# Kernel optimization log

Hardware: AMD Instinct MI355X
Metric: run time of the kernel (lower is better)

Reference implementation:

```python
import jax, jax.numpy as jnp
import numpy as np

N = 50000       # nodes
E = 800000      # edges (avg degree 16)
NFEAT = 256
NHID = 32
NHEADS = 4
ALPHA = 0.2     # leaky relu slope


def setup_inputs() -> dict:
    key = jax.random.key(0)
    ks = jax.random.split(key, 7)
    x = jax.random.normal(ks[0], (N, NFEAT), dtype=jnp.float32)
    src = jax.random.randint(ks[1], (E,), 0, N, dtype=jnp.int32)
    dst = jax.random.randint(ks[2], (E,), 0, N, dtype=jnp.int32)
    Ws = jax.random.normal(ks[3], (NHEADS, NFEAT, NHID), dtype=jnp.float32) * 0.05
    As = jax.random.normal(ks[4], (NHEADS, 2 * NHID), dtype=jnp.float32) * 0.05
    Wo = jax.random.normal(ks[5], (NHID * NHEADS, NHID), dtype=jnp.float32) * 0.05
    Ao = jax.random.normal(ks[6], (2 * NHID,), dtype=jnp.float32) * 0.05
    return {"x": x, "src": src, "dst": dst, "Ws": Ws, "As": As, "Wo": Wo, "Ao": Ao}


def _gat_layer(h, src, dst, W, a, concat):
    # h: [N, F_in] -> project
    h = h @ W                          # [N, d]
    d = W.shape[1]
    hs = h[src]                        # [E, d] gather source feats
    hd = h[dst]                        # [E, d] gather neighbor feats
    # a . concat([hs, hd]) == hs @ a[:d] + hd @ a[d:]
    e = hs @ a[:d] + hd @ a[d:]        # [E]
    e = jnp.where(e > 0, e, ALPHA * e)  # leaky relu
    # segment softmax keyed on src
    m = jax.ops.segment_max(e, src, num_segments=N)    # [N]
    ex = jnp.exp(e - m[src])
    denom = jax.ops.segment_sum(ex, src, num_segments=N)  # [N]
    att = ex / denom[src]              # [E]
    # weighted neighbor aggregation (scatter-sum on src)
    h_prime = jax.ops.segment_sum(att[:, None] * hd, src, num_segments=N)  # [N, d]
    return jax.nn.elu(h_prime) if concat else h_prime


def reference(x, src, dst, Ws, As, Wo, Ao):
    heads = [_gat_layer(x, src, dst, Ws[i], As[i], concat=True) for i in range(NHEADS)]
    h = jnp.concatenate(heads, axis=1)                 # [N, nhid*nheads]
    out = jax.nn.elu(_gat_layer(h, src, dst, Wo, Ao, concat=False))  # [N, nhid]
    return out
```

## Files before the change

kernel.cpp:

```cpp
#include <hip/hip_runtime.h>
#include <hip/hip_fp16.h>
#include <math.h>

#define N_NODES 50000
#define N_EDGES 800000
#define NFEAT 256
#define NHID 32
#define NHEADS 4
#define ALPHA 0.2f
#define ELLCAP 64
#define ELLSH 6

typedef _Float16 half8_t __attribute__((ext_vector_type(8)));
typedef float f32x4 __attribute__((ext_vector_type(4)));

__device__ __forceinline__ float elu_f(float x) {
    return x > 0.0f ? x : (__expf(x) - 1.0f);
}

__device__ __forceinline__ float wexp(float x) {
    float l = x > 0.0f ? x : ALPHA * x;
    return __expf(l);
}

__global__ void k_prep(const float* __restrict__ Ws, const float* __restrict__ Wo,
                       ushort* __restrict__ Wt1, ushort* __restrict__ Wt2) {
    int idx = blockIdx.x * 256 + threadIdx.x;
    if (idx < 128 * 256) {
        int c = idx >> 8;
        int k = idx & 255;
        __half hv = __float2half(Ws[(c >> 5) * (NFEAT * NHID) + k * NHID + (c & 31)]);
        Wt1[idx] = *(ushort*)&hv;
    } else if (idx < 128 * 256 + 32 * 128) {
        int j = idx - 128 * 256;
        int c = j >> 7;
        int k = j & 127;
        __half hv = __float2half(Wo[k * NHID + c]);
        Wt2[j] = *(ushort*)&hv;
    }
}

template <int K, int NTILES, bool AHALF, int NH>
__global__ __launch_bounds__(256) void k_gemm_mfma(const void* __restrict__ Ain,
                                                   const ushort* __restrict__ Wt,
                                                   const float* __restrict__ attn,
                                                   __half* __restrict__ C,
                                                   float* __restrict__ So,
                                                   float* __restrict__ Si,
                                                   int nrows) {
    constexpr int N = NTILES * 16;
    constexpr int BK = 32;
    constexpr int LDB = 40;

    __shared__ __align__(16) ushort Bs[N * LDB];

    int tid = threadIdx.x;
    int w = tid >> 6;
    int lane = tid & 63;
    int c = lane & 15;
    int quad = lane >> 4;
    int row0 = blockIdx.x * 64 + w * 16;
    int gm = row0 + c;
    if (gm >= nrows) gm = nrows - 1;

    f32x4 acc[NTILES];
#pragma unroll
    for (int nt = 0; nt < NTILES; nt++)
#pragma unroll
        for (int i = 0; i < 4; i++) acc[nt][i] = 0.0f;

    float a_so[NTILES], a_si[NTILES];
#pragma unroll
    for (int nt = 0; nt < NTILES; nt++) {
        int h = nt >> 1;
        a_so[nt] = attn[h * 64 + (nt & 1) * 16 + c];
        a_si[nt] = attn[h * 64 + 32 + (nt & 1) * 16 + c];
    }

    for (int k0 = 0; k0 < K; k0 += BK) {
        if (tid < N * 2) {
            int r = tid >> 1;
            int part = tid & 1;
            const uint4* gp = (const uint4*)(Wt + (size_t)r * K + k0 + part * 16);
            uint4 v0 = gp[0];
            uint4 v1 = gp[1];
            uint4* lp = (uint4*)&Bs[r * LDB + part * 16];
            lp[0] = v0;
            lp[1] = v1;
        }
        __syncthreads();

        half8_t ahi, alo;
        if constexpr (AHALF) {
            ahi = *(const half8_t*)((const ushort*)Ain + (size_t)gm * K + k0 + quad * 8);
        } else {
            const float* ap = (const float*)Ain + (size_t)gm * K + k0 + quad * 8;
            float4 x0 = *(const float4*)ap;
            float4 x1 = *(const float4*)(ap + 4);
            float xa[8] = {x0.x, x0.y, x0.z, x0.w, x1.x, x1.y, x1.z, x1.w};
#pragma unroll
            for (int j = 0; j < 8; j++) {
                _Float16 h = (_Float16)xa[j];
                ahi[j] = h;
                alo[j] = (_Float16)(xa[j] - (float)h);
            }
        }
#pragma unroll
        for (int nt = 0; nt < NTILES; nt++) {
            half8_t b = *(const half8_t*)&Bs[(nt * 16 + c) * LDB + quad * 8];
            acc[nt] = __builtin_amdgcn_mfma_f32_16x16x32_f16(ahi, b, acc[nt], 0, 0, 0);
            if constexpr (!AHALF)
                acc[nt] = __builtin_amdgcn_mfma_f32_16x16x32_f16(alo, b, acc[nt], 0, 0, 0);
        }
        __syncthreads();
    }

#pragma unroll
    for (int reg = 0; reg < 4; reg++) {
        int ro = row0 + quad * 4 + reg;
        bool ok = ro < nrows;
        if (ok) {
#pragma unroll
            for (int nt = 0; nt < NTILES; nt++)
                C[(size_t)ro * N + nt * 16 + c] = __float2half(acc[nt][reg]);
        }
#pragma unroll
        for (int h = 0; h < NH; h++) {
            float so = acc[2 * h][reg] * a_so[2 * h] + acc[2 * h + 1][reg] * a_so[2 * h + 1];
            float si = acc[2 * h][reg] * a_si[2 * h] + acc[2 * h + 1][reg] * a_si[2 * h + 1];
            so += __shfl_xor(so, 1); si += __shfl_xor(si, 1);
            so += __shfl_xor(so, 2); si += __shfl_xor(si, 2);
            so += __shfl_xor(so, 4); si += __shfl_xor(si, 4);
            so += __shfl_xor(so, 8); si += __shfl_xor(si, 8);
            if (c == 0 && ok) {
                So[(size_t)ro * NH + h] = so;
                Si[(size_t)ro * NH + h] = si;
            }
        }
    }
}

__global__ void k_fill(const int* __restrict__ src, const int* __restrict__ dst,
                       int* __restrict__ deg, int* __restrict__ ell) {
    int e = blockIdx.x * 256 + threadIdx.x;
    if (e >= N_EDGES) return;
    int s = src[e];
    int v = dst[e];
    int slot = atomicAdd(&deg[s], 1);
    if (slot < ELLCAP) ell[((size_t)s << ELLSH) + slot] = v;
}

__global__ __launch_bounds__(256) void k_aggw4(const int* __restrict__ deg,
                                               const int* __restrict__ ell,
                                               const float* __restrict__ S1o,
                                               const float* __restrict__ S1i,
                                               const __half* __restrict__ H1h,
                                               __half* __restrict__ Hch) {
    int node = blockIdx.x * 4 + (threadIdx.x >> 6);
    if (node >= N_NODES) return;
    int lane = threadIdx.x & 63;
    int ha = lane >> 4;
    int dg = deg[node];
    if (dg > ELLCAP) dg = ELLCAP;
    const int* lp = ell + ((size_t)node << ELLSH);
    const unsigned* Hp = (const unsigned*)H1h;
    float so = S1o[node * 4 + ha];
    float a0 = 0.0f, a1 = 0.0f, d = 0.0f;
    int j = 0;
    for (; j + 1 < dg; j += 2) {
        int v0 = lp[j];
        int v1 = lp[j + 1];
        float w0 = wexp(so + S1i[4 * (size_t)v0 + ha]);
        float w1 = wexp(so + S1i[4 * (size_t)v1 + ha]);
        unsigned u0 = Hp[((size_t)v0 << 6) + lane];
        unsigned u1 = Hp[((size_t)v1 << 6) + lane];
        float2 h0 = __half22float2(*(__half2*)&u0);
        float2 h1 = __half22float2(*(__half2*)&u1);
        a0 += w0 * h0.x; a1 += w0 * h0.y; d += w0;
        a0 += w1 * h1.x; a1 += w1 * h1.y; d += w1;
    }
    if (j < dg) {
        int v0 = lp[j];
        float w0 = wexp(so + S1i[4 * (size_t)v0 + ha]);
        unsigned u0 = Hp[((size_t)v0 << 6) + lane];
        float2 h0 = __half22float2(*(__half2*)&u0);
        a0 += w0 * h0.x; a1 += w0 * h0.y; d += w0;
    }
    float inv = d > 0.0f ? 1.0f / d : 0.0f;
    __half2 o = __floats2half2_rn(elu_f(a0 * inv), elu_f(a1 * inv));
    *(__half2*)(Hch + ((size_t)node << 7) + 2 * lane) = o;
}

__global__ __launch_bounds__(256) void k_aggw2(const int* __restrict__ deg,
                                               const int* __restrict__ ell,
                                               const float* __restrict__ S2o,
                                               const float* __restrict__ S2i,
                                               const __half* __restrict__ H2h,
                                               float* __restrict__ out) {
    int t = blockIdx.x * 256 + threadIdx.x;
    int node = t >> 4;
    if (node >= N_NODES) return;
    int l = t & 15;
    int dg = deg[node];
    if (dg > ELLCAP) dg = ELLCAP;
    const int* lp = ell + ((size_t)node << ELLSH);
    const unsigned* Hp = (const unsigned*)H2h;
    float so = S2o[node];
    float a0 = 0.0f, a1 = 0.0f, d = 0.0f;
    int j = 0;
    for (; j + 1 < dg; j += 2) {
        int v0 = lp[j];
        int v1 = lp[j + 1];
        float w0 = wexp(so + S2i[v0]);
        float w1 = wexp(so + S2i[v1]);
        unsigned u0 = Hp[((size_t)v0 << 4) + l];
        unsigned u1 = Hp[((size_t)v1 << 4) + l];
        float2 h0 = __half22float2(*(__half2*)&u0);
        float2 h1 = __half22float2(*(__half2*)&u1);
        a0 += w0 * h0.x; a1 += w0 * h0.y; d += w0;
        a0 += w1 * h1.x; a1 += w1 * h1.y; d += w1;
    }
    if (j < dg) {
        int v0 = lp[j];
        float w0 = wexp(so + S2i[v0]);
        unsigned u0 = Hp[((size_t)v0 << 4) + l];
        float2 h0 = __half22float2(*(__half2*)&u0);
        a0 += w0 * h0.x; a1 += w0 * h0.y; d += w0;
    }
    float inv = d > 0.0f ? 1.0f / d : 0.0f;
    float2 o = make_float2(elu_f(a0 * inv), elu_f(a1 * inv));
    *(float2*)(out + ((size_t)node << 5) + 2 * l) = o;
}

extern "C" void kernel_launch(void* const* d_in, const int* in_sizes, int n_in,
                              void* d_out, int out_size, void* d_ws, size_t ws_size,
                              hipStream_t stream) {
    const float* x = (const float*)d_in[0];
    const int* src = (const int*)d_in[1];
    const int* dst = (const int*)d_in[2];
    const float* Ws = (const float*)d_in[3];
    const float* As = (const float*)d_in[4];
    const float* Wo = (const float*)d_in[5];
    const float* Ao = (const float*)d_in[6];
    float* out = (float*)d_out;

    char* p = (char*)d_ws;
    auto alloc = [&](size_t bytes) -> void* {
        void* r = (void*)p;
        p += (bytes + 255) & ~(size_t)255;
        return r;
    };
    ushort* Wt1 = (ushort*)alloc((size_t)128 * 256 * 2);
    ushort* Wt2 = (ushort*)alloc((size_t)32 * 128 * 2);
    __half* H1h = (__half*)alloc((size_t)N_NODES * 128 * 2);
    __half* Hch = (__half*)alloc((size_t)N_NODES * 128 * 2);
    __half* H2h = (__half*)alloc((size_t)N_NODES * 32 * 2);
    float* S1o = (float*)alloc((size_t)N_NODES * 4 * 4);
    float* S1i = (float*)alloc((size_t)N_NODES * 4 * 4);
    float* S2o = (float*)alloc((size_t)N_NODES * 4);
    float* S2i = (float*)alloc((size_t)N_NODES * 4);
    int* deg   = (int*)alloc((size_t)N_NODES * 4);
    int* ell   = (int*)alloc((size_t)N_NODES * ELLCAP * 4);

    const int EDGE_BLKS = (N_EDGES + 255) / 256;
    const int GEMM_BLKS = (N_NODES + 63) / 64;

    hipMemsetAsync(deg, 0, (size_t)N_NODES * 4, stream);

    k_prep<<<(128 * 256 + 32 * 128 + 255) / 256, 256, 0, stream>>>(Ws, Wo, Wt1, Wt2);

    k_gemm_mfma<256, 8, false, 4><<<GEMM_BLKS, 256, 0, stream>>>(
        x, Wt1, As, H1h, S1o, S1i, N_NODES);

    k_fill<<<EDGE_BLKS, 256, 0, stream>>>(src, dst, deg, ell);

    k_aggw4<<<(N_NODES + 3) / 4, 256, 0, stream>>>(deg, ell, S1o, S1i, H1h, Hch);

    k_gemm_mfma<128, 2, true, 1><<<GEMM_BLKS, 256, 0, stream>>>(
        Hch, Wt2, Ao, H2h, S2o, S2i, N_NODES);

    k_aggw2<<<(N_NODES * 16 + 255) / 256, 256, 0, stream>>>(deg, ell, S2o, S2i, H2h, out);
}
```

Measured before the change: 242.2 us.

## Precompute per-edge attention weights in fill pass, store with neighbor in ELL

The fill kernel now computes the four layer-1 attention exponentials per edge, packed as halves, and stores them next to the neighbor index in a 16-byte ELL entry. A new edge pass does the same for layer 2, writing into the reused H1h buffer. Both aggregation kernels then read the weights directly instead of gathering S*i and calling exp for each neighbor, and their loops unroll by 4. In exchange the ELL footprint grows (16B and 8B per entry), an extra edge kernel and an eslot array are added, and the layer-1 weights drop to half precision.

Measured after the change: 243.7 us. About the same (+0.6%).

```diff
diff --git a/kernel.cpp b/kernel.cpp
--- a/kernel.cpp
+++ b/kernel.cpp
@@ -21,6 +21,11 @@
 __device__ __forceinline__ float wexp(float x) {
     float l = x > 0.0f ? x : ALPHA * x;
     return __expf(l);
+}
+
+__device__ __forceinline__ float h2f_bits(unsigned wd, int sh) {
+    ushort b = (ushort)(wd >> sh);
+    return __half2float(*(__half*)&b);
 }
 
 __global__ void k_prep(const float* __restrict__ Ws, const float* __restrict__ Wo,
@@ -141,48 +146,70 @@
 }
 
 __global__ void k_fill(const int* __restrict__ src, const int* __restrict__ dst,
-                       int* __restrict__ deg, int* __restrict__ ell) {
+                       const float* __restrict__ S1o, const float* __restrict__ S1i,
+                       int* __restrict__ deg, uint4* __restrict__ ell16,
+                       int* __restrict__ eslot) {
     int e = blockIdx.x * 256 + threadIdx.x;
     if (e >= N_EDGES) return;
     int s = src[e];
     int v = dst[e];
     int slot = atomicAdd(&deg[s], 1);
-    if (slot < ELLCAP) ell[((size_t)s << ELLSH) + slot] = v;
+    eslot[e] = slot;
+    if (slot >= ELLCAP) return;
+    float4 so = *(const float4*)(S1o + 4 * (size_t)s);
+    float4 si = *(const float4*)(S1i + 4 * (size_t)v);
+    __half2 w01 = __floats2half2_rn(wexp(so.x + si.x), wexp(so.y + si.y));
+    __half2 w23 = __floats2half2_rn(wexp(so.z + si.z), wexp(so.w + si.w));
+    uint4 q;
+    q.x = (unsigned)v;
+    q.y = *(unsigned*)&w01;
+    q.z = *(unsigned*)&w23;
+    q.w = 0;
+    ell16[((size_t)s << ELLSH) + slot] = q;
 }
 
 __global__ __launch_bounds__(256) void k_aggw4(const int* __restrict__ deg,
-                                               const int* __restrict__ ell,
-                                               const float* __restrict__ S1o,
-                                               const float* __restrict__ S1i,
+                                               const uint4* __restrict__ ell16,
                                                const __half* __restrict__ H1h,
                                                __half* __restrict__ Hch) {
     int node = blockIdx.x * 4 + (threadIdx.x >> 6);
     if (node >= N_NODES) return;
     int lane = threadIdx.x & 63;
     int ha = lane >> 4;
+    int sel = ha & 2;
+    int sh = (ha & 1) * 16;
     int dg = deg[node];
     if (dg > ELLCAP) dg = ELLCAP;
-    const int* lp = ell + ((size_t)node << ELLSH);
+    const uint4* lp = ell16 + ((size_t)node << ELLSH);
     const unsigned* Hp = (const unsigned*)H1h;
-    float so = S1o[node * 4 + ha];
     float a0 = 0.0f, a1 = 0.0f, d = 0.0f;
     int j = 0;
-    for (; j + 1 < dg; j += 2) {
-        int v0 = lp[j];
-        int v1 = lp[j + 1];
-        float w0 = wexp(so + S1i[4 * (size_t)v0 + ha]);
-        float w1 = wexp(so + S1i[4 * (size_t)v1 + ha]);
-        unsigned u0 = Hp[((size_t)v0 << 6) + lane];
-        unsigned u1 = Hp[((size_t)v1 << 6) + lane];
+    for (; j + 3 < dg; j += 4) {
+        uint4 q0 = lp[j];
+        uint4 q1 = lp[j + 1];
+        uint4 q2 = lp[j + 2];
+        uint4 q3 = lp[j + 3];
+        unsigned u0 = Hp[((size_t)q0.x << 6) + lane];
+        unsigned u1 = Hp[((size_t)q1.x << 6) + lane];
+        unsigned u2 = Hp[((size_t)q2.x << 6) + lane];
+        unsigned u3 = Hp[((size_t)q3.x << 6) + lane];
+        float w0 = h2f_bits(sel ? q0.z : q0.y, sh);
+        float w1 = h2f_bits(sel ? q1.z : q1.y, sh);
+        float w2 = h2f_bits(sel ? q2.z : q2.y, sh);
+        float w3 = h2f_bits(sel ? q3.z : q3.y, sh);
         float2 h0 = __half22float2(*(__half2*)&u0);
         float2 h1 = __half22float2(*(__half2*)&u1);
+        float2 h2 = __half22float2(*(__half2*)&u2);
+        float2 h3 = __half22float2(*(__half2*)&u3);
         a0 += w0 * h0.x; a1 += w0 * h0.y; d += w0;
         a0 += w1 * h1.x; a1 += w1 * h1.y; d += w1;
-    }
-    if (j < dg) {
-        int v0 = lp[j];
-        float w0 = wexp(so + S1i[4 * (size_t)v0 + ha]);
-        unsigned u0 = Hp[((size_t)v0 << 6) + lane];
+        a0 += w2 * h2.x; a1 += w2 * h2.y; d += w2;
+        a0 += w3 * h3.x; a1 += w3 * h3.y; d += w3;
+    }
+    for (; j < dg; j++) {
+        uint4 q0 = lp[j];
+        unsigned u0 = Hp[((size_t)q0.x << 6) + lane];
+        float w0 = h2f_bits(sel ? q0.z : q0.y, sh);
         float2 h0 = __half22float2(*(__half2*)&u0);
         a0 += w0 * h0.x; a1 += w0 * h0.y; d += w0;
     }
@@ -191,10 +218,25 @@
     *(__half2*)(Hch + ((size_t)node << 7) + 2 * lane) = o;
 }
 
+__global__ void k_w2fill(const int* __restrict__ src, const int* __restrict__ dst,
+                         const int* __restrict__ eslot,
+                         const float* __restrict__ S2o, const float* __restrict__ S2i,
+                         uint2* __restrict__ ew2) {
+    int e = blockIdx.x * 256 + threadIdx.x;
+    if (e >= N_EDGES) return;
+    int s = src[e];
+    int v = dst[e];
+    int slot = eslot[e];
+    if (slot >= ELLCAP) return;
+    float w = wexp(S2o[s] + S2i[v]);
+    uint2 q;
+    q.x = (unsigned)v;
+    q.y = __float_as_uint(w);
+    ew2[((size_t)s << ELLSH) + slot] = q;
+}
+
 __global__ __launch_bounds__(256) void k_aggw2(const int* __restrict__ deg,
-                                               const int* __restrict__ ell,
-                                               const float* __restrict__ S2o,
-                                               const float* __restrict__ S2i,
+                                               const uint2* __restrict__ ew2,
                                                const __half* __restrict__ H2h,
                                                float* __restrict__ out) {
     int t = blockIdx.x * 256 + threadIdx.x;
@@ -203,27 +245,36 @@
     int l = t & 15;
     int dg = deg[node];
     if (dg > ELLCAP) dg = ELLCAP;
-    const int* lp = ell + ((size_t)node << ELLSH);
+    const uint2* lp = ew2 + ((size_t)node << ELLSH);
     const unsigned* Hp = (const unsigned*)H2h;
-    float so = S2o[node];
     float a0 = 0.0f, a1 = 0.0f, d = 0.0f;
     int j = 0;
-    for (; j + 1 < dg; j += 2) {
-        int v0 = lp[j];
-        int v1 = lp[j + 1];
-        float w0 = wexp(so + S2i[v0]);
-        float w1 = wexp(so + S2i[v1]);
-        unsigned u0 = Hp[((size_t)v0 << 4) + l];
-        unsigned u1 = Hp[((size_t)v1 << 4) + l];
+    for (; j + 3 < dg; j += 4) {
+        uint2 q0 = lp[j];
+        uint2 q1 = lp[j + 1];
+        uint2 q2 = lp[j + 2];
+        uint2 q3 = lp[j + 3];
+        unsigned u0 = Hp[((size_t)q0.x << 4) + l];
+        unsigned u1 = Hp[((size_t)q1.x << 4) + l];
+        unsigned u2 = Hp[((size_t)q2.x << 4) + l];
+        unsigned u3 = Hp[((size_t)q3.x << 4) + l];
+        float w0 = __uint_as_float(q0.y);
+        float w1 = __uint_as_float(q1.y);
+        float w2 = __uint_as_float(q2.y);
+        float w3 = __uint_as_float(q3.y);
         float2 h0 = __half22float2(*(__half2*)&u0);
         float2 h1 = __half22float2(*(__half2*)&u1);
+        float2 h2 = __half22float2(*(__half2*)&u2);
+        float2 h3 = __half22float2(*(__half2*)&u3);
         a0 += w0 * h0.x; a1 += w0 * h0.y; d += w0;
         a0 += w1 * h1.x; a1 += w1 * h1.y; d += w1;
-    }
-    if (j < dg) {
-        int v0 = lp[j];
-        float w0 = wexp(so + S2i[v0]);
-        unsigned u0 = Hp[((size_t)v0 << 4) + l];
+        a0 += w2 * h2.x; a1 += w2 * h2.y; d += w2;
+        a0 += w3 * h3.x; a1 += w3 * h3.y; d += w3;
+    }
+    for (; j < dg; j++) {
+        uint2 q0 = lp[j];
+        unsigned u0 = Hp[((size_t)q0.x << 4) + l];
+        float w0 = __uint_as_float(q0.y);
         float2 h0 = __half22float2(*(__half2*)&u0);
         a0 += w0 * h0.x; a1 += w0 * h0.y; d += w0;
     }
@@ -254,13 +305,15 @@
     ushort* Wt2 = (ushort*)alloc((size_t)32 * 128 * 2);
     __half* H1h = (__half*)alloc((size_t)N_NODES * 128 * 2);
     __half* Hch = (__half*)alloc((size_t)N_NODES * 128 * 2);
+    uint2* ew2 = (uint2*)H1h;
     __half* H2h = (__half*)alloc((size_t)N_NODES * 32 * 2);
     float* S1o = (float*)alloc((size_t)N_NODES * 4 * 4);
     float* S1i = (float*)alloc((size_t)N_NODES * 4 * 4);
     float* S2o = (float*)alloc((size_t)N_NODES * 4);
     float* S2i = (float*)alloc((size_t)N_NODES * 4);
     int* deg   = (int*)alloc((size_t)N_NODES * 4);
-    int* ell   = (int*)alloc((size_t)N_NODES * ELLCAP * 4);
+    int* eslot = (int*)alloc((size_t)N_EDGES * 4);
+    uint4* ell16 = (uint4*)alloc((size_t)N_NODES * ELLCAP * 16);
 
     const int EDGE_BLKS = (N_EDGES + 255) / 256;
     const int GEMM_BLKS = (N_NODES + 63) / 64;
@@ -272,12 +325,14 @@
     k_gemm_mfma<256, 8, false, 4><<<GEMM_BLKS, 256, 0, stream>>>(
         x, Wt1, As, H1h, S1o, S1i, N_NODES);
 
-    k_fill<<<EDGE_BLKS, 256, 0, stream>>>(src, dst, deg, ell);
-
-    k_aggw4<<<(N_NODES + 3) / 4, 256, 0, stream>>>(deg, ell, S1o, S1i, H1h, Hch);
+    k_fill<<<EDGE_BLKS, 256, 0, stream>>>(src, dst, S1o, S1i, deg, ell16, eslot);
+
+    k_aggw4<<<(N_NODES + 3) / 4, 256, 0, stream>>>(deg, ell16, H1h, Hch);
 
     k_gemm_mfma<128, 2, true, 1><<<GEMM_BLKS, 256, 0, stream>>>(
         Hch, Wt2, Ao, H2h, S2o, S2i, N_NODES);
 
-    k_aggw2<<<(N_NODES * 16 + 255) / 256, 256, 0, stream>>>(deg, ell, S2o, S2i, H2h, out);
-}
+    k_w2fill<<<EDGE_BLKS, 256, 0, stream>>>(src, dst, eslot, S2o, S2i, ew2);
+
+    k_aggw2<<<(N_NODES * 16 + 255) / 256, 256, 0, stream>>>(deg, ew2, H2h, out);
+}
```

## Precompute per-edge attention weights into ELL-aligned buffers before aggregation

Applied to the files above, without the earlier changes.

Adds two per-slot kernels that compute the leaky-relu exp attention weights once per edge: packed fp16 for the four heads in layer 1, fp32 for layer 2. They are stored alongside the ELL neighbor list. The aggregation kernels then read neighbors and weights with vectorized 16-byte loads and unroll by four, no longer doing redundant per-lane score gathers and exps. The cost is two extra launches over all 64 slots per node, extra workspace traffic for the weight arrays, and fp16 rounding of the layer-1 weights.

Result: no change. 245.0 us (+1.2%).

```diff
diff --git a/kernel.cpp b/kernel.cpp
--- a/kernel.cpp
+++ b/kernel.cpp
@@ -21,6 +21,11 @@
 __device__ __forceinline__ float wexp(float x) {
     float l = x > 0.0f ? x : ALPHA * x;
     return __expf(l);
+}
+
+__device__ __forceinline__ float h2f_bits(unsigned wd, int sh) {
+    ushort b = (ushort)(wd >> sh);
+    return __half2float(*(__half*)&b);
 }
 
 __global__ void k_prep(const float* __restrict__ Ws, const float* __restrict__ Wo,
@@ -141,48 +146,82 @@
 }
 
 __global__ void k_fill(const int* __restrict__ src, const int* __restrict__ dst,
-                       int* __restrict__ deg, int* __restrict__ ell) {
+                       int* __restrict__ deg, int* __restrict__ ell4) {
     int e = blockIdx.x * 256 + threadIdx.x;
     if (e >= N_EDGES) return;
     int s = src[e];
     int v = dst[e];
     int slot = atomicAdd(&deg[s], 1);
-    if (slot < ELLCAP) ell[((size_t)s << ELLSH) + slot] = v;
+    if (slot < ELLCAP) ell4[((size_t)s << ELLSH) + slot] = v;
+}
+
+__global__ __launch_bounds__(256) void k_wfill1(const int* __restrict__ deg,
+                                                const int* __restrict__ ell4,
+                                                const float* __restrict__ S1o,
+                                                const float* __restrict__ S1i,
+                                                uint2* __restrict__ ellw8) {
+    int t = blockIdx.x * 256 + threadIdx.x;
+    int node = t >> ELLSH;
+    if (node >= N_NODES) return;
+    int slot = t & (ELLCAP - 1);
+    int dg = deg[node];
+    if (dg > ELLCAP) dg = ELLCAP;
+    if (slot >= dg) return;
+    int v = ell4[t];
+    float4 so = *(const float4*)(S1o + 4 * (size_t)node);
+    float4 si = *(const float4*)(S1i + 4 * (size_t)v);
+    __half2 w01 = __floats2half2_rn(wexp(so.x + si.x), wexp(so.y + si.y));
+    __half2 w23 = __floats2half2_rn(wexp(so.z + si.z), wexp(so.w + si.w));
+    uint2 q;
+    q.x = *(unsigned*)&w01;
+    q.y = *(unsigned*)&w23;
+    ellw8[t] = q;
 }
 
 __global__ __launch_bounds__(256) void k_aggw4(const int* __restrict__ deg,
-                                               const int* __restrict__ ell,
-                                               const float* __restrict__ S1o,
-                                               const float* __restrict__ S1i,
+                                               const int* __restrict__ ell4,
+                                               const uint2* __restrict__ ellw8,
                                                const __half* __restrict__ H1h,
                                                __half* __restrict__ Hch) {
     int node = blockIdx.x * 4 + (threadIdx.x >> 6);
     if (node >= N_NODES) return;
     int lane = threadIdx.x & 63;
     int ha = lane >> 4;
+    int sel = ha & 2;
+    int sh = (ha & 1) * 16;
     int dg = deg[node];
     if (dg > ELLCAP) dg = ELLCAP;
-    const int* lp = ell + ((size_t)node << ELLSH);
+    const uint4* dp = (const uint4*)(ell4 + ((size_t)node << ELLSH));
+    const uint4* wp = (const uint4*)(ellw8 + ((size_t)node << ELLSH));
     const unsigned* Hp = (const unsigned*)H1h;
-    float so = S1o[node * 4 + ha];
     float a0 = 0.0f, a1 = 0.0f, d = 0.0f;
     int j = 0;
-    for (; j + 1 < dg; j += 2) {
-        int v0 = lp[j];
-        int v1 = lp[j + 1];
-        float w0 = wexp(so + S1i[4 * (size_t)v0 + ha]);
-        float w1 = wexp(so + S1i[4 * (size_t)v1 + ha]);
-        unsigned u0 = Hp[((size_t)v0 << 6) + lane];
-        unsigned u1 = Hp[((size_t)v1 << 6) + lane];
+    for (; j + 3 < dg; j += 4) {
+        uint4 d4 = dp[j >> 2];
+        uint4 wA = wp[j >> 1];
+        uint4 wB = wp[(j >> 1) + 1];
+        unsigned u0 = Hp[((size_t)d4.x << 6) + lane];
+        unsigned u1 = Hp[((size_t)d4.y << 6) + lane];
+        unsigned u2 = Hp[((size_t)d4.z << 6) + lane];
+        unsigned u3 = Hp[((size_t)d4.w << 6) + lane];
+        float w0 = h2f_bits(sel ? wA.y : wA.x, sh);
+        float w1 = h2f_bits(sel ? wA.w : wA.z, sh);
+        float w2 = h2f_bits(sel ? wB.y : wB.x, sh);
+        float w3 = h2f_bits(sel ? wB.w : wB.z, sh);
         float2 h0 = __half22float2(*(__half2*)&u0);
         float2 h1 = __half22float2(*(__half2*)&u1);
+        float2 h2 = __half22float2(*(__half2*)&u2);
+        float2 h3 = __half22float2(*(__half2*)&u3);
         a0 += w0 * h0.x; a1 += w0 * h0.y; d += w0;
         a0 += w1 * h1.x; a1 += w1 * h1.y; d += w1;
-    }
-    if (j < dg) {
-        int v0 = lp[j];
-        float w0 = wexp(so + S1i[4 * (size_t)v0 + ha]);
+        a0 += w2 * h2.x; a1 += w2 * h2.y; d += w2;
+        a0 += w3 * h3.x; a1 += w3 * h3.y; d += w3;
+    }
+    for (; j < dg; j++) {
+        int v0 = ell4[((size_t)node << ELLSH) + j];
+        uint2 q0 = ellw8[((size_t)node << ELLSH) + j];
         unsigned u0 = Hp[((size_t)v0 << 6) + lane];
+        float w0 = h2f_bits(sel ? q0.y : q0.x, sh);
         float2 h0 = __half22float2(*(__half2*)&u0);
         a0 += w0 * h0.x; a1 += w0 * h0.y; d += w0;
     }
@@ -191,10 +230,25 @@
     *(__half2*)(Hch + ((size_t)node << 7) + 2 * lane) = o;
 }
 
+__global__ __launch_bounds__(256) void k_wfill2(const int* __restrict__ deg,
+                                                const int* __restrict__ ell4,
+                                                const float* __restrict__ S2o,
+                                                const float* __restrict__ S2i,
+                                                float* __restrict__ ew2) {
+    int t = blockIdx.x * 256 + threadIdx.x;
+    int node = t >> ELLSH;
+    if (node >= N_NODES) return;
+    int slot = t & (ELLCAP - 1);
+    int dg = deg[node];
+    if (dg > ELLCAP) dg = ELLCAP;
+    if (slot >= dg) return;
+    int v = ell4[t];
+    ew2[t] = wexp(S2o[node] + S2i[v]);
+}
+
 __global__ __launch_bounds__(256) void k_aggw2(const int* __restrict__ deg,
-                                               const int* __restrict__ ell,
-                                               const float* __restrict__ S2o,
-                                               const float* __restrict__ S2i,
+                                               const int* __restrict__ ell4,
+                                               const float* __restrict__ ew2,
                                                const __half* __restrict__ H2h,
                                                float* __restrict__ out) {
     int t = blockIdx.x * 256 + threadIdx.x;
@@ -203,26 +257,30 @@
     int l = t & 15;
     int dg = deg[node];
     if (dg > ELLCAP) dg = ELLCAP;
-    const int* lp = ell + ((size_t)node << ELLSH);
+    const uint4* dp = (const uint4*)(ell4 + ((size_t)node << ELLSH));
+    const f32x4* wp = (const f32x4*)(ew2 + ((size_t)node << ELLSH));
     const unsigned* Hp = (const unsigned*)H2h;
-    float so = S2o[node];
     float a0 = 0.0f, a1 = 0.0f, d = 0.0f;
     int j = 0;
-    for (; j + 1 < dg; j += 2) {
-        int v0 = lp[j];
-        int v1 = lp[j + 1];
-        float w0 = wexp(so + S2i[v0]);
-        float w1 = wexp(so + S2i[v1]);
-        unsigned u0 = Hp[((size_t)v0 << 4) + l];
-        unsigned u1 = Hp[((size_t)v1 << 4) + l];
+    for (; j + 3 < dg; j += 4) {
+        uint4 d4 = dp[j >> 2];
+        f32x4 w4 = wp[j >> 2];
+        unsigned u0 = Hp[((size_t)d4.x << 4) + l];
+        unsigned u1 = Hp[((size_t)d4.y << 4) + l];
+        unsigned u2 = Hp[((size_t)d4.z << 4) + l];
+        unsigned u3 = Hp[((size_t)d4.w << 4) + l];
         float2 h0 = __half22float2(*(__half2*)&u0);
         float2 h1 = __half22float2(*(__half2*)&u1);
-        a0 += w0 * h0.x; a1 += w0 * h0.y; d += w0;
-        a0 += w1 * h1.x; a1 += w1 * h1.y; d += w1;
-    }
-    if (j < dg) {
-        int v0 = lp[j];
-        float w0 = wexp(so + S2i[v0]);
+        float2 h2 = __half22float2(*(__half2*)&u2);
+        float2 h3 = __half22float2(*(__half2*)&u3);
+        a0 += w4[0] * h0.x; a1 += w4[0] * h0.y; d += w4[0];
+        a0 += w4[1] * h1.x; a1 += w4[1] * h1.y; d += w4[1];
+        a0 += w4[2] * h2.x; a1 += w4[2] * h2.y; d += w4[2];
+        a0 += w4[3] * h3.x; a1 += w4[3] * h3.y; d += w4[3];
+    }
+    for (; j < dg; j++) {
+        int v0 = ell4[((size_t)node << ELLSH) + j];
+        float w0 = ew2[((size_t)node << ELLSH) + j];
         unsigned u0 = Hp[((size_t)v0 << 4) + l];
         float2 h0 = __half22float2(*(__half2*)&u0);
         a0 += w0 * h0.x; a1 += w0 * h0.y; d += w0;
@@ -260,10 +318,13 @@
     float* S2o = (float*)alloc((size_t)N_NODES * 4);
     float* S2i = (float*)alloc((size_t)N_NODES * 4);
     int* deg   = (int*)alloc((size_t)N_NODES * 4);
-    int* ell   = (int*)alloc((size_t)N_NODES * ELLCAP * 4);
+    int* ell4  = (int*)alloc((size_t)N_NODES * ELLCAP * 4);
+    uint2* ellw8 = (uint2*)alloc((size_t)N_NODES * ELLCAP * 8);
+    float* ew2 = (float*)ellw8;
 
     const int EDGE_BLKS = (N_EDGES + 255) / 256;
     const int GEMM_BLKS = (N_NODES + 63) / 64;
+    const int SLOT_BLKS = (N_NODES * ELLCAP + 255) / 256;
 
     hipMemsetAsync(deg, 0, (size_t)N_NODES * 4, stream);
 
@@ -272,12 +333,16 @@
     k_gemm_mfma<256, 8, false, 4><<<GEMM_BLKS, 256, 0, stream>>>(
         x, Wt1, As, H1h, S1o, S1i, N_NODES);
 
-    k_fill<<<EDGE_BLKS, 256, 0, stream>>>(src, dst, deg, ell);
-
-    k_aggw4<<<(N_NODES + 3) / 4, 256, 0, stream>>>(deg, ell, S1o, S1i, H1h, Hch);
+    k_fill<<<EDGE_BLKS, 256, 0, stream>>>(src, dst, deg, ell4);
+
+    k_wfill1<<<SLOT_BLKS, 256, 0, stream>>>(deg, ell4, S1o, S1i, ellw8);
+
+    k_aggw4<<<(N_NODES + 3) / 4, 256, 0, stream>>>(deg, ell4, ellw8, H1h, Hch);
 
     k_gemm_mfma<128, 2, true, 1><<<GEMM_BLKS, 256, 0, stream>>>(
         Hch, Wt2, Ao, H2h, S2o, S2i, N_NODES);
 
-    k_aggw2<<<(N_NODES * 16 + 255) / 256, 256, 0, stream>>>(deg, ell, S2o, S2i, H2h, out);
-}
+    k_wfill2<<<SLOT_BLKS, 256, 0, stream>>>(deg, ell4, S2o, S2i, ew2);
+
+    k_aggw2<<<(N_NODES * 16 + 255) / 256, 256, 0, stream>>>(deg, ell4, ew2, H2h, out);
+}
```
